# Performance work log

Hardware: AMD Instinct MI355X
Metric: run time of the kernel (lower is better)

The kernel has to match this reference:

```python
import jax, jax.numpy as jnp
import numpy as np

EMBED_DIM = 1280
NUM_HEADS = 20
HEAD_DIM = EMBED_DIM // NUM_HEADS
BSZ, SEQ = 4, 1500


def setup_inputs() -> dict:
    key = jax.random.key(0)
    ks = jax.random.split(key, 8)
    s = 1.0 / np.sqrt(EMBED_DIM)
    return {
        "hidden_states": jax.random.normal(ks[0], (BSZ, SEQ, EMBED_DIM), jnp.float32),
        "attention_mask": jnp.zeros((BSZ, 1, SEQ, SEQ), jnp.float32),
        "Wq": jax.random.normal(ks[1], (EMBED_DIM, EMBED_DIM), jnp.float32) * s,
        "bq": jax.random.normal(ks[2], (EMBED_DIM,), jnp.float32) * 0.01,
        "Wk": jax.random.normal(ks[3], (EMBED_DIM, EMBED_DIM), jnp.float32) * s,
        "Wv": jax.random.normal(ks[4], (EMBED_DIM, EMBED_DIM), jnp.float32) * s,
        "bv": jax.random.normal(ks[5], (EMBED_DIM,), jnp.float32) * 0.01,
        "Wo": jax.random.normal(ks[6], (EMBED_DIM, EMBED_DIM), jnp.float32) * s,
        "bo": jax.random.normal(ks[7], (EMBED_DIM,), jnp.float32) * 0.01,
    }


def _split_heads(x):
    b, s, _ = x.shape
    return x.reshape(b, s, NUM_HEADS, HEAD_DIM).transpose(0, 2, 1, 3)  # [b,h,s,d]


def reference(hidden_states, attention_mask, Wq, bq, Wk, Wv, bv, Wo, bo):
    scale = jnp.float32(HEAD_DIM) ** -0.5
    q = (hidden_states @ Wq.T + bq) * scale          # [b,s,e]
    k = hidden_states @ Wk.T                          # k_proj has no bias
    v = hidden_states @ Wv.T + bv
    q, k, v = _split_heads(q), _split_heads(k), _split_heads(v)
    attn = jnp.einsum("bhqd,bhkd->bhqk", q, k)       # [b,h,s,s]
    attn = attn + attention_mask
    attn = jax.nn.softmax(attn, axis=-1)
    out = jnp.einsum("bhqk,bhkd->bhqd", attn, v)     # [b,h,s,d]
    out = out.transpose(0, 2, 1, 3).reshape(hidden_states.shape)
    return out @ Wo.T + bo
```

## Files before the change

### kernel.cpp

```cpp
#include <hip/hip_runtime.h>

typedef unsigned short u16;
typedef unsigned long long u64;
using bf16x8 = __attribute__((ext_vector_type(8))) __bf16;
using f32x4  = __attribute__((ext_vector_type(4))) float;
using u32x2  = __attribute__((ext_vector_type(2))) unsigned;
using u32x4  = __attribute__((ext_vector_type(4))) unsigned;

#define AS1 __attribute__((address_space(1)))
#define AS3 __attribute__((address_space(3)))

__device__ __forceinline__ void glds16(const u16* g, u16* l) {
  __builtin_amdgcn_global_load_lds((AS1 void*)const_cast<u16*>(g), (AS3 void*)l, 16, 0, 0);
}

__device__ __forceinline__ u16 f2bf(float f) {
  unsigned u = __float_as_uint(f);
  u += 0x7FFFu + ((u >> 16) & 1u);
  return (u16)(u >> 16);
}
__device__ __forceinline__ ushort4 cvt4(float4 v) {
  return make_ushort4(f2bf(v.x), f2bf(v.y), f2bf(v.z), f2bf(v.w));
}

__device__ __forceinline__ unsigned cvt_pk_bf16(float lo, float hi) {
  unsigned r;
  asm("v_cvt_pk_bf16_f32 %0, %1, %2" : "=v"(r) : "v"(lo), "v"(hi));
  return r;
}

#if __has_builtin(__builtin_amdgcn_exp2f)
__device__ __forceinline__ float fexp2(float x) { return __builtin_amdgcn_exp2f(x); }
#else
__device__ __forceinline__ float fexp2(float x) { return exp2f(x); }
#endif

__device__ __forceinline__ void quad_swap(unsigned& x, unsigned& y) {
  u32x2 a = __builtin_amdgcn_permlane32_swap(x, y, false, false);
  u32x2 b = __builtin_amdgcn_permlane16_swap(a[0], a[1], false, false);
  x = b[0];
  y = b[1];
}

__device__ __forceinline__ float xquad_max(float x) {
  u32x2 a = __builtin_amdgcn_permlane16_swap(__float_as_uint(x), __float_as_uint(x), false, false);
  float y = fmaxf(__uint_as_float(a[0]), __uint_as_float(a[1]));
  u32x2 b = __builtin_amdgcn_permlane32_swap(__float_as_uint(y), __float_as_uint(y), false, false);
  return fmaxf(__uint_as_float(b[0]), __uint_as_float(b[1]));
}
__device__ __forceinline__ float xquad_sum(float x) {
  u32x2 a = __builtin_amdgcn_permlane16_swap(__float_as_uint(x), __float_as_uint(x), false, false);
  float y = __uint_as_float(a[0]) + __uint_as_float(a[1]);
  u32x2 b = __builtin_amdgcn_permlane32_swap(__float_as_uint(y), __float_as_uint(y), false, false);
  return __uint_as_float(b[0]) + __uint_as_float(b[1]);
}

__global__ __launch_bounds__(256) void cvt_kernel(const float4* __restrict__ hs,
    const float4* __restrict__ wq, const float4* __restrict__ wk,
    const float4* __restrict__ wv, const float4* __restrict__ wo, u16* __restrict__ dst) {
  const long stride = (long)gridDim.x * blockDim.x;
  for (long i = (long)blockIdx.x * blockDim.x + threadIdx.x; i < 3558400; i += stride) {
    const float4* src; long rel; u16* d;
    if (i < 1920000)      { src = hs; rel = i;           d = dst; }
    else if (i < 2329600) { src = wq; rel = i - 1920000; d = dst + 7680000; }
    else if (i < 2739200) { src = wk; rel = i - 2329600; d = dst + 9318400; }
    else if (i < 3148800) { src = wv; rel = i - 2739200; d = dst + 10956800; }
    else                  { src = wo; rel = i - 3148800; d = dst + 12595200; }
    *(ushort4*)(d + rel * 4) = cvt4(src[rel]);
  }
}

template <int MODE, typename OT>
__device__ __forceinline__ void gemm256(const u16* __restrict__ A, const u16* __restrict__ W,
                                        const float* __restrict__ bias, OT* __restrict__ out,
                                        float scale, int M, u16* lds, int m0, int n0) {
  constexpr int K = 1280;
  constexpr int NT = 20;
  const int tid = threadIdx.x, wid = tid >> 6, lane = tid & 63;
  const int lm = lane & 15, quad = lane >> 4;
  const int wr = wid >> 1, wc = wid & 1;

  f32x4 acc[4][4] = {};

  const int srow = tid >> 3, sslot = tid & 7;
  const int scol = (sslot ^ (srow & 7)) * 8;
  int r0 = m0 + srow;       r0 = r0 < M ? r0 : M - 1;
  int r1 = m0 + 64 + srow;  r1 = r1 < M ? r1 : M - 1;
  int r2 = m0 + 128 + srow; r2 = r2 < M ? r2 : M - 1;
  int r3 = m0 + 192 + srow; r3 = r3 < M ? r3 : M - 1;
  const u16* a0 = A + (size_t)r0 * K + scol;
  const u16* a1 = A + (size_t)r1 * K + scol;
  const u16* a2 = A + (size_t)r2 * K + scol;
  const u16* a3 = A + (size_t)r3 * K + scol;
  const u16* w0 = W + (size_t)(n0 + srow) * K + scol;
  const u16* w1 = W + (size_t)(n0 + 64 + srow) * K + scol;
  const int wdst = wid * 512;

  auto stage_p = [&](int t, int bsel2, int p) {
    u16* bb = lds + bsel2 * 24576;
    const int kt = t * 64;
    if (p == 0) {
      glds16(a0 + kt, bb + wdst);
      glds16(a1 + kt, bb + 4096 + wdst);
      glds16(a2 + kt, bb + 8192 + wdst);
    } else {
      glds16(a3 + kt, bb + 12288 + wdst);
      glds16(w0 + kt, bb + 16384 + wdst);
      glds16(w1 + kt, bb + 20480 + wdst);
    }
  };

  stage_p(0, 0, 0); stage_p(0, 0, 1);
  stage_p(1, 1, 0); stage_p(1, 1, 1);
  asm volatile("s_waitcnt vmcnt(6)" ::: "memory");
  __builtin_amdgcn_s_barrier();

  int bsel = 0;
  for (int t = 0; t < NT; ++t) {
    const u16* Ab = lds + bsel * 24576;
    const u16* Bb = Ab + 16384;
    const int b2 = bsel >= 1 ? bsel - 1 : 2;
    const bool pf = (t + 2) < NT;
#pragma unroll
    for (int kk = 0; kk < 2; ++kk) {
      const int co = ((kk * 4 + quad) ^ (lm & 7)) * 8;
      bf16x8 af[4], bfr[4];
#pragma unroll
      for (int i = 0; i < 4; ++i)
        af[i] = *(const bf16x8*)(Ab + (wr * 64 + i * 16 + lm) * 64 + co);
#pragma unroll
      for (int j = 0; j < 4; ++j)
        bfr[j] = *(const bf16x8*)(Bb + (wc * 64 + j * 16 + lm) * 64 + co);
      if (pf) stage_p(t + 2, b2, kk);
      __builtin_amdgcn_sched_barrier(0);
      __builtin_amdgcn_s_barrier();
      __builtin_amdgcn_s_setprio(1);
#pragma unroll
      for (int i = 0; i < 4; ++i)
#pragma unroll
        for (int j = 0; j < 4; ++j)
          acc[i][j] = __builtin_amdgcn_mfma_f32_16x16x32_bf16(af[i], bfr[j], acc[i][j], 0, 0, 0);
      __builtin_amdgcn_s_setprio(0);
      __builtin_amdgcn_s_barrier();
    }
    if (t + 1 < NT) {
      if (pf) asm volatile("s_waitcnt vmcnt(6)" ::: "memory");
      else    asm volatile("s_waitcnt vmcnt(0)" ::: "memory");
      __builtin_amdgcn_s_barrier();
    }
    bsel = bsel == 2 ? 0 : bsel + 1;
  }

  if constexpr (MODE == 2) {
    __syncthreads();
    u16* Ct = lds;
#pragma unroll
    for (int j = 0; j < 4; ++j) {
      const int col = wc * 64 + j * 16 + lm;
      const float bb = bias ? bias[n0 + col] : 0.0f;
#pragma unroll
      for (int i = 0; i < 4; ++i) {
        const int row = wr * 64 + i * 16 + quad * 4;
        ushort4 pk;
        pk.x = f2bf((acc[i][j][0] + bb) * scale);
        pk.y = f2bf((acc[i][j][1] + bb) * scale);
        pk.z = f2bf((acc[i][j][2] + bb) * scale);
        pk.w = f2bf((acc[i][j][3] + bb) * scale);
        *(ushort4*)(Ct + col * 264 + row) = pk;
      }
    }
    __syncthreads();
#pragma unroll
    for (int k = 0; k < 8; ++k) {
      const int c8 = tid + k * 512;
      const int col = c8 >> 5, rc = c8 & 31;
      const int grow0 = m0 + rc * 8;
      if (grow0 >= M) continue;
      const int gcol = n0 + col, hh = gcol >> 6, dd = gcol & 63;
      const u16* src = Ct + col * 264 + rc * 8;
      const int b0 = grow0 / 1500, b1 = (grow0 + 7) / 1500;
      if (b0 == b1) {
        const int s = grow0 - b0 * 1500;
        u16* dst = (u16*)out + ((size_t)((b0 * 20 + hh) * 64 + dd)) * 1504 + s;
        *(u64*)dst = *(const u64*)src;
        *(u64*)(dst + 4) = *(const u64*)(src + 4);
      } else {
#pragma unroll
        for (int r = 0; r < 8; ++r) {
          const int g = grow0 + r;
          const int bi2 = g / 1500, s2 = g - bi2 * 1500;
          ((u16*)out)[((size_t)((bi2 * 20 + hh) * 64 + dd)) * 1504 + s2] = src[r];
        }
      }
    }
  } else {
#pragma unroll
    for (int j = 0; j < 4; ++j) {
      const int col = n0 + wc * 64 + j * 16 + lm;
      const float bb = bias ? bias[col] : 0.0f;
      const int hh = col >> 6, dd = col & 63;
#pragma unroll
      for (int i = 0; i < 4; ++i) {
        const int row0 = m0 + wr * 64 + i * 16 + quad * 4;
#pragma unroll
        for (int r = 0; r < 4; ++r) {
          const int row = row0 + r;
          if (row < M) {
            const float v = (acc[i][j][r] + bb) * scale;
            if (MODE == 0) {
              out[(size_t)row * 1280 + col] = (OT)v;
            } else {
              const int bidx = row / 1500, s = row - bidx * 1500;
              out[((size_t)(bidx * 20 + hh) * 1500 + s) * 64 + dd] = (OT)f2bf(v);
            }
          }
        }
      }
    }
  }
}

__global__ __launch_bounds__(512, 2) void qkv_kernel(const u16* __restrict__ hs,
    const u16* __restrict__ Wq, const float* __restrict__ bq, const u16* __restrict__ Wk,
    const u16* __restrict__ Wv, const float* __restrict__ bv,
    u16* __restrict__ q_ws, u16* __restrict__ k_ws, u16* __restrict__ vt_ws, int M) {
  __shared__ __align__(16) u16 lds[3 * 24576];
  const int n = blockIdx.x;
  const int xcd = n & 7, j = n >> 3;
  const int x = xcd * 3 + (j % 3);
  const int yz = j / 3;
  const int y = yz % 10, z = yz / 10;
  const int m0 = x * 256, n0 = y * 128;
  if (z == 0)
    gemm256<1, u16>(hs, Wq, bq, q_ws, 0.18033688f, M, lds, m0, n0);
  else if (z == 1)
    gemm256<1, u16>(hs, Wk, nullptr, k_ws, 1.0f, M, lds, m0, n0);
  else
    gemm256<2, u16>(hs, Wv, bv, vt_ws, 1.0f, M, lds, m0, n0);
}

__global__ __launch_bounds__(512, 2) void out_kernel(const u16* __restrict__ attn,
    const u16* __restrict__ Wo, const float* __restrict__ bo, float* __restrict__ out, int M) {
  __shared__ __align__(16) u16 lds[3 * 24576];
  const int n = blockIdx.x;
  const int xcd = n & 7, j = n >> 3;
  const int x = xcd * 3 + (j % 3);
  const int y = j / 3;
  gemm256<0, float>(attn, Wo, bo, out, 1.0f, M, lds, x * 256, y * 128);
}

__global__ __launch_bounds__(256, 3) void attn_kernel(const u16* __restrict__ Qm,
    const u16* __restrict__ Km, const u16* __restrict__ Vtm, u16* __restrict__ Out) {
  const int n = blockIdx.x;
  const int xcd = n & 7, j = n >> 3;
  const int bh = xcd * 10 + (j % 10);
  const int qt = j / 10;
  const int b = bh / 20, h = bh % 20;
  const int tid = threadIdx.x, wid = tid >> 6, lane = tid & 63;
  const int lm = lane & 15, quad = lane >> 4;

  __shared__ __align__(16) u16 lds[3 * 8192];

  const u16* Qb = Qm + (size_t)bh * (1500 * 64);
  const u16* Kb = Km + (size_t)bh * (1500 * 64);
  const u16* Vb = Vtm + (size_t)bh * (64 * 1504);

  bf16x8 qf[2][2];
#pragma unroll
  for (int g = 0; g < 2; ++g) {
    int qrow = qt * 128 + wid * 32 + g * 16 + lm;
    if (qrow > 1499) qrow = 1499;
    qf[g][0] = *(const bf16x8*)(Qb + (size_t)qrow * 64 + quad * 8);
    qf[g][1] = *(const bf16x8*)(Qb + (size_t)qrow * 64 + 32 + quad * 8);
  }

  const int rr = tid >> 3, cc = tid & 7;
  const int s0 = (cc ^ (rr & 7)) * 8;

  auto stage = [&](int kt, int bi) {
    int kr0 = kt + rr;      if (kr0 > 1499) kr0 = 1499;
    int kr1 = kt + rr + 32; if (kr1 > 1499) kr1 = 1499;
    int vcol = kt + s0;     if (vcol > 1496) vcol = 1496;
    u16* lk = lds + bi * 8192 + wid * 512;
    u16* lv = lk + 4096;
    glds16(Kb + (size_t)kr0 * 64 + s0, lk);
    glds16(Kb + (size_t)kr1 * 64 + s0, lk + 2048);
    glds16(Vb + (size_t)rr * 1504 + vcol, lv);
    glds16(Vb + (size_t)(rr + 32) * 1504 + vcol, lv + 2048);
  };

  stage(0, 0);
  stage(64, 1);
  asm volatile("s_waitcnt vmcnt(4)" ::: "memory");
  __builtin_amdgcn_s_barrier();

  float m_s[2] = {-1e30f, -1e30f};
  float l_s[2] = {0.f, 0.f};
  f32x4 o_acc[2][4] = {};

  int bsel = 0;
  for (int it = 0; it < 24; ++it) {
    const u16* Kc = lds + bsel * 8192;
    const u16* Vc = Kc + 4096;
    if (it + 2 < 24) stage((it + 2) * 64, bsel >= 1 ? bsel - 1 : 2);

    f32x4 st[2][4] = {};
    __builtin_amdgcn_s_setprio(1);
#pragma unroll
    for (int kk = 0; kk < 2; ++kk) {
#pragma unroll
      for (int t = 0; t < 4; ++t) {
        const bf16x8 kf = *(const bf16x8*)(Kc + (t * 16 + lm) * 64 + (((kk * 4 + quad) ^ (lm & 7)) * 8));
        st[0][t] = __builtin_amdgcn_mfma_f32_16x16x32_bf16(kf, qf[0][kk], st[0][t], 0, 0, 0);
        st[1][t] = __builtin_amdgcn_mfma_f32_16x16x32_bf16(kf, qf[1][kk], st[1][t], 0, 0, 0);
      }
    }
    __builtin_amdgcn_s_setprio(0);
    if (it == 23) {
#pragma unroll
      for (int t = 0; t < 4; ++t)
#pragma unroll
        for (int r = 0; r < 4; ++r)
          if (t * 16 + quad * 4 + r >= 28) { st[0][t][r] = -1e30f; st[1][t][r] = -1e30f; }
    }

    bf16x8 pf[2][2];
#pragma unroll
    for (int g = 0; g < 2; ++g) {
      float a0 = fmaxf(fmaxf(st[g][0][0], st[g][0][1]), fmaxf(st[g][0][2], st[g][0][3]));
      float a1 = fmaxf(fmaxf(st[g][1][0], st[g][1][1]), fmaxf(st[g][1][2], st[g][1][3]));
      float a2 = fmaxf(fmaxf(st[g][2][0], st[g][2][1]), fmaxf(st[g][2][2], st[g][2][3]));
      float a3 = fmaxf(fmaxf(st[g][3][0], st[g][3][1]), fmaxf(st[g][3][2], st[g][3][3]));
      float rm = xquad_max(fmaxf(fmaxf(a0, a1), fmaxf(a2, a3)));

      if (!__all(rm - m_s[g] <= 8.0f)) {
        const float mn = fmaxf(m_s[g], rm);
        const float al = fexp2(m_s[g] - mn);
        m_s[g] = mn;
        l_s[g] *= al;
#pragma unroll
        for (int r = 0; r < 4; ++r) {
          const float ao = __shfl(al, quad * 4 + r);
#pragma unroll
          for (int t = 0; t < 4; ++t) o_acc[g][t][r] *= ao;
        }
      }
      const float mn = m_s[g];

      float rs = 0.f;
      unsigned A[4], B[4];
#pragma unroll
      for (int t = 0; t < 4; ++t) {
        const float p0 = fexp2(st[g][t][0] - mn);
        const float p1 = fexp2(st[g][t][1] - mn);
        const float p2 = fexp2(st[g][t][2] - mn);
        const float p3 = fexp2(st[g][t][3] - mn);
        rs += (p0 + p1) + (p2 + p3);
        A[t] = cvt_pk_bf16(p0, p1);
        B[t] = cvt_pk_bf16(p2, p3);
      }
      l_s[g] += xquad_sum(rs);

#pragma unroll
      for (int kk = 0; kk < 2; ++kk) {
        unsigned x0 = A[2 * kk], x1 = A[2 * kk + 1];
        quad_swap(x0, x1);
        unsigned y0 = B[2 * kk], y1 = B[2 * kk + 1];
        quad_swap(y0, y1);
        u32x4 w; w[0] = x0; w[1] = y0; w[2] = x1; w[3] = y1;
        pf[g][kk] = __builtin_bit_cast(bf16x8, w);
      }
    }

    __builtin_amdgcn_s_setprio(1);
#pragma unroll
    for (int kk = 0; kk < 2; ++kk) {
#pragma unroll
      for (int t = 0; t < 4; ++t) {
        const bf16x8 vf = *(const bf16x8*)(Vc + (t * 16 + lm) * 64 + (((kk * 4 + quad) ^ (lm & 7)) * 8));
        o_acc[0][t] = __builtin_amdgcn_mfma_f32_16x16x32_bf16(pf[0][kk], vf, o_acc[0][t], 0, 0, 0);
        o_acc[1][t] = __builtin_amdgcn_mfma_f32_16x16x32_bf16(pf[1][kk], vf, o_acc[1][t], 0, 0, 0);
      }
    }
    __builtin_amdgcn_s_setprio(0);

    if (it + 1 < 24) {
      if (it + 2 < 24) asm volatile("s_waitcnt vmcnt(4)" ::: "memory");
      else             asm volatile("s_waitcnt vmcnt(0)" ::: "memory");
      __builtin_amdgcn_s_barrier();
    }
    bsel = bsel == 2 ? 0 : bsel + 1;
  }

#pragma unroll
  for (int g = 0; g < 2; ++g)
#pragma unroll
    for (int r = 0; r < 4; ++r) {
      const float lr = __shfl(l_s[g], quad * 4 + r);
      const float inv = 1.0f / lr;
      const int qg = qt * 128 + wid * 32 + g * 16 + quad * 4 + r;
      if (qg < 1500) {
#pragma unroll
        for (int t = 0; t < 4; ++t)
          Out[((size_t)(b * 1500 + qg)) * 1280 + h * 64 + t * 16 + lm] =
              f2bf(o_acc[g][t][r] * inv);
      }
    }
}

extern "C" void kernel_launch(void* const* d_in, const int* in_sizes, int n_in,
                              void* d_out, int out_size, void* d_ws, size_t ws_size,
                              hipStream_t stream) {
  const float* hs = (const float*)d_in[0];
  const float* Wq = (const float*)d_in[2];
  const float* bq = (const float*)d_in[3];
  const float* Wk = (const float*)d_in[4];
  const float* Wv = (const float*)d_in[5];
  const float* bv = (const float*)d_in[6];
  const float* Wo = (const float*)d_in[7];
  const float* bo = (const float*)d_in[8];

  u16* cvt     = (u16*)d_ws;
  u16* hs_bf   = cvt;
  u16* Wq_bf   = cvt + 7680000;
  u16* Wk_bf   = cvt + 9318400;
  u16* Wv_bf   = cvt + 10956800;
  u16* Wo_bf   = cvt + 12595200;
  u16* q_ws    = cvt + 14233600;
  u16* k_ws    = q_ws + 7680000;
  u16* vt_ws   = k_ws + 7680000;
  u16* attn_ws = vt_ws + 7700480 + 64;
  const int M = 6000;

  hipLaunchKernelGGL(cvt_kernel, dim3(2048), dim3(256), 0, stream,
                     (const float4*)hs, (const float4*)Wq, (const float4*)Wk,
                     (const float4*)Wv, (const float4*)Wo, cvt);
  hipLaunchKernelGGL(qkv_kernel, dim3(720), dim3(512), 0, stream,
                     hs_bf, Wq_bf, bq, Wk_bf, Wv_bf, bv, q_ws, k_ws, vt_ws, M);
  hipLaunchKernelGGL(attn_kernel, dim3(960), dim3(256), 0, stream,
                     q_ws, k_ws, vt_ws, attn_ws);
  hipLaunchKernelGGL(out_kernel, dim3(240), dim3(512), 0, stream,
                     attn_ws, Wo_bf, bo, (float*)d_out, M);
}
```

Baseline: 312.5 us.

## Enlarge GEMM tiles to 256x256 with an 8-phase double-buffered pipeline

Replaces the 256x128 triple-buffered GEMM with a 256x256 tile. Each of 8 waves now computes 128x64 (8x4 MFMA accumulators), and loads are interleaved over four compute phases using two LDS buffers. This halves the grid sizes for the QKV and output projections, aiming to raise arithmetic intensity and reduce LDS/global traffic per FLOP. The cost is more accumulator registers, fewer blocks for the 256 CUs (360 and 120), and a V-transpose epilogue split into two column chunks.

Result: slower. 341.7 us (+9.3%).

```diff
diff --git a/kernel.cpp b/kernel.cpp
--- a/kernel.cpp
+++ b/kernel.cpp
@@ -71,125 +71,178 @@
 }
 
 template <int MODE, typename OT>
-__device__ __forceinline__ void gemm256(const u16* __restrict__ A, const u16* __restrict__ W,
-                                        const float* __restrict__ bias, OT* __restrict__ out,
-                                        float scale, int M, u16* lds, int m0, int n0) {
+__device__ __forceinline__ void gemm8p(const u16* __restrict__ A, const u16* __restrict__ W,
+                                       const float* __restrict__ bias, OT* __restrict__ out,
+                                       float scale, int M, u16* lds, int m0, int n0) {
   constexpr int K = 1280;
   constexpr int NT = 20;
   const int tid = threadIdx.x, wid = tid >> 6, lane = tid & 63;
   const int lm = lane & 15, quad = lane >> 4;
-  const int wr = wid >> 1, wc = wid & 1;
-
-  f32x4 acc[4][4] = {};
+  const int wr = wid >> 2, wc = wid & 3;
+
+  f32x4 acc[8][4] = {};
 
   const int srow = tid >> 3, sslot = tid & 7;
   const int scol = (sslot ^ (srow & 7)) * 8;
-  int r0 = m0 + srow;       r0 = r0 < M ? r0 : M - 1;
-  int r1 = m0 + 64 + srow;  r1 = r1 < M ? r1 : M - 1;
-  int r2 = m0 + 128 + srow; r2 = r2 < M ? r2 : M - 1;
-  int r3 = m0 + 192 + srow; r3 = r3 < M ? r3 : M - 1;
-  const u16* a0 = A + (size_t)r0 * K + scol;
-  const u16* a1 = A + (size_t)r1 * K + scol;
-  const u16* a2 = A + (size_t)r2 * K + scol;
-  const u16* a3 = A + (size_t)r3 * K + scol;
-  const u16* w0 = W + (size_t)(n0 + srow) * K + scol;
-  const u16* w1 = W + (size_t)(n0 + 64 + srow) * K + scol;
+  const u16* ap[4]; const u16* wp[4];
+#pragma unroll
+  for (int i = 0; i < 4; ++i) {
+    int ra = m0 + i * 64 + srow; ra = ra < M ? ra : M - 1;
+    ap[i] = A + (size_t)ra * K + scol;
+    wp[i] = W + (size_t)(n0 + i * 64 + srow) * K + scol;
+  }
   const int wdst = wid * 512;
 
-  auto stage_p = [&](int t, int bsel2, int p) {
-    u16* bb = lds + bsel2 * 24576;
+  auto stA = [&](int t, int b, int half) {
     const int kt = t * 64;
-    if (p == 0) {
-      glds16(a0 + kt, bb + wdst);
-      glds16(a1 + kt, bb + 4096 + wdst);
-      glds16(a2 + kt, bb + 8192 + wdst);
-    } else {
-      glds16(a3 + kt, bb + 12288 + wdst);
-      glds16(w0 + kt, bb + 16384 + wdst);
-      glds16(w1 + kt, bb + 20480 + wdst);
-    }
+    glds16(ap[2 * half] + kt,     lds + b * 32768 + (2 * half) * 4096 + wdst);
+    glds16(ap[2 * half + 1] + kt, lds + b * 32768 + (2 * half + 1) * 4096 + wdst);
   };
-
-  stage_p(0, 0, 0); stage_p(0, 0, 1);
-  stage_p(1, 1, 0); stage_p(1, 1, 1);
-  asm volatile("s_waitcnt vmcnt(6)" ::: "memory");
+  auto stB = [&](int t, int b, int half) {
+    const int kt = t * 64;
+    glds16(wp[2 * half] + kt,     lds + b * 32768 + 16384 + (2 * half) * 4096 + wdst);
+    glds16(wp[2 * half + 1] + kt, lds + b * 32768 + 16384 + (2 * half + 1) * 4096 + wdst);
+  };
+
+  stA(0, 0, 0); stA(0, 0, 1); stB(0, 0, 0); stB(0, 0, 1);
+  stA(1, 1, 0); stB(1, 1, 0);
+  asm volatile("s_waitcnt vmcnt(4)" ::: "memory");
   __builtin_amdgcn_s_barrier();
 
-  int bsel = 0;
   for (int t = 0; t < NT; ++t) {
-    const u16* Ab = lds + bsel * 24576;
+    const int b = t & 1;
+    const u16* Ab = lds + b * 32768;
     const u16* Bb = Ab + 16384;
-    const int b2 = bsel >= 1 ? bsel - 1 : 2;
-    const bool pf = (t + 2) < NT;
-#pragma unroll
-    for (int kk = 0; kk < 2; ++kk) {
-      const int co = ((kk * 4 + quad) ^ (lm & 7)) * 8;
-      bf16x8 af[4], bfr[4];
+    const int co0 = ((0 + quad) ^ (lm & 7)) * 8;
+    const int co1 = ((4 + quad) ^ (lm & 7)) * 8;
+    bf16x8 afh[2][4], bf[2][4];
+
+#pragma unroll
+    for (int i = 0; i < 4; ++i) {
+      afh[0][i] = *(const bf16x8*)(Ab + (wr * 128 + i * 16 + lm) * 64 + co0);
+      afh[1][i] = *(const bf16x8*)(Ab + (wr * 128 + i * 16 + lm) * 64 + co1);
+    }
+#pragma unroll
+    for (int j = 0; j < 2; ++j) {
+      bf[0][j] = *(const bf16x8*)(Bb + (wc * 64 + j * 16 + lm) * 64 + co0);
+      bf[1][j] = *(const bf16x8*)(Bb + (wc * 64 + j * 16 + lm) * 64 + co1);
+    }
+    if (t + 1 < NT) stA(t + 1, b ^ 1, 1);
+    __builtin_amdgcn_sched_barrier(0);
+    __builtin_amdgcn_s_barrier();
+    __builtin_amdgcn_s_setprio(1);
+#pragma unroll
+    for (int kk = 0; kk < 2; ++kk)
 #pragma unroll
       for (int i = 0; i < 4; ++i)
-        af[i] = *(const bf16x8*)(Ab + (wr * 64 + i * 16 + lm) * 64 + co);
-#pragma unroll
-      for (int j = 0; j < 4; ++j)
-        bfr[j] = *(const bf16x8*)(Bb + (wc * 64 + j * 16 + lm) * 64 + co);
-      if (pf) stage_p(t + 2, b2, kk);
-      __builtin_amdgcn_sched_barrier(0);
-      __builtin_amdgcn_s_barrier();
-      __builtin_amdgcn_s_setprio(1);
+#pragma unroll
+        for (int j = 0; j < 2; ++j)
+          acc[i][j] = __builtin_amdgcn_mfma_f32_16x16x32_bf16(afh[kk][i], bf[kk][j], acc[i][j], 0, 0, 0);
+    __builtin_amdgcn_s_setprio(0);
+    __builtin_amdgcn_s_barrier();
+
+#pragma unroll
+    for (int j = 2; j < 4; ++j) {
+      bf[0][j] = *(const bf16x8*)(Bb + (wc * 64 + j * 16 + lm) * 64 + co0);
+      bf[1][j] = *(const bf16x8*)(Bb + (wc * 64 + j * 16 + lm) * 64 + co1);
+    }
+    if (t + 1 < NT) stB(t + 1, b ^ 1, 1);
+    __builtin_amdgcn_sched_barrier(0);
+    __builtin_amdgcn_s_barrier();
+    __builtin_amdgcn_s_setprio(1);
+#pragma unroll
+    for (int kk = 0; kk < 2; ++kk)
 #pragma unroll
       for (int i = 0; i < 4; ++i)
 #pragma unroll
-        for (int j = 0; j < 4; ++j)
-          acc[i][j] = __builtin_amdgcn_mfma_f32_16x16x32_bf16(af[i], bfr[j], acc[i][j], 0, 0, 0);
-      __builtin_amdgcn_s_setprio(0);
-      __builtin_amdgcn_s_barrier();
-    }
+        for (int j = 2; j < 4; ++j)
+          acc[i][j] = __builtin_amdgcn_mfma_f32_16x16x32_bf16(afh[kk][i], bf[kk][j], acc[i][j], 0, 0, 0);
+    __builtin_amdgcn_s_setprio(0);
+    __builtin_amdgcn_s_barrier();
+
+#pragma unroll
+    for (int i = 0; i < 4; ++i) {
+      afh[0][i] = *(const bf16x8*)(Ab + (wr * 128 + (i + 4) * 16 + lm) * 64 + co0);
+      afh[1][i] = *(const bf16x8*)(Ab + (wr * 128 + (i + 4) * 16 + lm) * 64 + co1);
+    }
+    if (t + 2 < NT) stA(t + 2, b, 0);
+    __builtin_amdgcn_sched_barrier(0);
+    __builtin_amdgcn_s_barrier();
+    __builtin_amdgcn_s_setprio(1);
+#pragma unroll
+    for (int kk = 0; kk < 2; ++kk)
+#pragma unroll
+      for (int i = 0; i < 4; ++i)
+#pragma unroll
+        for (int j = 0; j < 2; ++j)
+          acc[i + 4][j] = __builtin_amdgcn_mfma_f32_16x16x32_bf16(afh[kk][i], bf[kk][j], acc[i + 4][j], 0, 0, 0);
+    __builtin_amdgcn_s_setprio(0);
+    __builtin_amdgcn_s_barrier();
+
+    if (t + 2 < NT) stB(t + 2, b, 0);
+    __builtin_amdgcn_sched_barrier(0);
+    __builtin_amdgcn_s_barrier();
+    __builtin_amdgcn_s_setprio(1);
+#pragma unroll
+    for (int kk = 0; kk < 2; ++kk)
+#pragma unroll
+      for (int i = 0; i < 4; ++i)
+#pragma unroll
+        for (int j = 2; j < 4; ++j)
+          acc[i + 4][j] = __builtin_amdgcn_mfma_f32_16x16x32_bf16(afh[kk][i], bf[kk][j], acc[i + 4][j], 0, 0, 0);
+    __builtin_amdgcn_s_setprio(0);
     if (t + 1 < NT) {
-      if (pf) asm volatile("s_waitcnt vmcnt(6)" ::: "memory");
-      else    asm volatile("s_waitcnt vmcnt(0)" ::: "memory");
-      __builtin_amdgcn_s_barrier();
-    }
-    bsel = bsel == 2 ? 0 : bsel + 1;
+      if (t + 2 < NT) asm volatile("s_waitcnt vmcnt(4)" ::: "memory");
+      else            asm volatile("s_waitcnt vmcnt(0)" ::: "memory");
+    }
+    __builtin_amdgcn_s_barrier();
   }
 
   if constexpr (MODE == 2) {
-    __syncthreads();
     u16* Ct = lds;
 #pragma unroll
-    for (int j = 0; j < 4; ++j) {
-      const int col = wc * 64 + j * 16 + lm;
-      const float bb = bias ? bias[n0 + col] : 0.0f;
-#pragma unroll
-      for (int i = 0; i < 4; ++i) {
-        const int row = wr * 64 + i * 16 + quad * 4;
-        ushort4 pk;
-        pk.x = f2bf((acc[i][j][0] + bb) * scale);
-        pk.y = f2bf((acc[i][j][1] + bb) * scale);
-        pk.z = f2bf((acc[i][j][2] + bb) * scale);
-        pk.w = f2bf((acc[i][j][3] + bb) * scale);
-        *(ushort4*)(Ct + col * 264 + row) = pk;
-      }
-    }
-    __syncthreads();
-#pragma unroll
-    for (int k = 0; k < 8; ++k) {
-      const int c8 = tid + k * 512;
-      const int col = c8 >> 5, rc = c8 & 31;
-      const int grow0 = m0 + rc * 8;
-      if (grow0 >= M) continue;
-      const int gcol = n0 + col, hh = gcol >> 6, dd = gcol & 63;
-      const u16* src = Ct + col * 264 + rc * 8;
-      const int b0 = grow0 / 1500, b1 = (grow0 + 7) / 1500;
-      if (b0 == b1) {
-        const int s = grow0 - b0 * 1500;
-        u16* dst = (u16*)out + ((size_t)((b0 * 20 + hh) * 64 + dd)) * 1504 + s;
-        *(u64*)dst = *(const u64*)src;
-        *(u64*)(dst + 4) = *(const u64*)(src + 4);
-      } else {
-#pragma unroll
-        for (int r = 0; r < 8; ++r) {
-          const int g = grow0 + r;
-          const int bi2 = g / 1500, s2 = g - bi2 * 1500;
-          ((u16*)out)[((size_t)((bi2 * 20 + hh) * 64 + dd)) * 1504 + s2] = src[r];
+    for (int ch = 0; ch < 2; ++ch) {
+      __syncthreads();
+      if ((wc >> 1) == ch) {
+        const int colbase = (wc & 1) * 64;
+#pragma unroll
+        for (int j = 0; j < 4; ++j) {
+          const int col = colbase + j * 16 + lm;
+          const float bb = bias ? bias[n0 + ch * 128 + col] : 0.0f;
+#pragma unroll
+          for (int i = 0; i < 8; ++i) {
+            const int row = wr * 128 + i * 16 + quad * 4;
+            ushort4 pk;
+            pk.x = f2bf((acc[i][j][0] + bb) * scale);
+            pk.y = f2bf((acc[i][j][1] + bb) * scale);
+            pk.z = f2bf((acc[i][j][2] + bb) * scale);
+            pk.w = f2bf((acc[i][j][3] + bb) * scale);
+            *(ushort4*)(Ct + col * 264 + row) = pk;
+          }
+        }
+      }
+      __syncthreads();
+#pragma unroll
+      for (int k = 0; k < 8; ++k) {
+        const int c8 = tid + k * 512;
+        const int col = c8 >> 5, rc = c8 & 31;
+        const int grow0 = m0 + rc * 8;
+        if (grow0 >= M) continue;
+        const int gcol = n0 + ch * 128 + col, hh = gcol >> 6, dd = gcol & 63;
+        const u16* src = Ct + col * 264 + rc * 8;
+        const int b0 = grow0 / 1500, b1 = (grow0 + 7) / 1500;
+        if (b0 == b1) {
+          const int s = grow0 - b0 * 1500;
+          u16* dst = (u16*)out + ((size_t)((b0 * 20 + hh) * 64 + dd)) * 1504 + s;
+          *(u64*)dst = *(const u64*)src;
+          *(u64*)(dst + 4) = *(const u64*)(src + 4);
+        } else {
+#pragma unroll
+          for (int r = 0; r < 8; ++r) {
+            const int g = grow0 + r;
+            const int bi2 = g / 1500, s2 = g - bi2 * 1500;
+            ((u16*)out)[((size_t)((bi2 * 20 + hh) * 64 + dd)) * 1504 + s2] = src[r];
+          }
         }
       }
     }
@@ -200,8 +253,8 @@
       const float bb = bias ? bias[col] : 0.0f;
       const int hh = col >> 6, dd = col & 63;
 #pragma unroll
-      for (int i = 0; i < 4; ++i) {
-        const int row0 = m0 + wr * 64 + i * 16 + quad * 4;
+      for (int i = 0; i < 8; ++i) {
+        const int row0 = m0 + wr * 128 + i * 16 + quad * 4;
 #pragma unroll
         for (int r = 0; r < 4; ++r) {
           const int row = row0 + r;
@@ -224,29 +277,29 @@
     const u16* __restrict__ Wq, const float* __restrict__ bq, const u16* __restrict__ Wk,
     const u16* __restrict__ Wv, const float* __restrict__ bv,
     u16* __restrict__ q_ws, u16* __restrict__ k_ws, u16* __restrict__ vt_ws, int M) {
-  __shared__ __align__(16) u16 lds[3 * 24576];
+  __shared__ __align__(16) u16 lds[2 * 32768];
   const int n = blockIdx.x;
   const int xcd = n & 7, j = n >> 3;
   const int x = xcd * 3 + (j % 3);
   const int yz = j / 3;
-  const int y = yz % 10, z = yz / 10;
-  const int m0 = x * 256, n0 = y * 128;
+  const int y = yz % 5, z = yz / 5;
+  const int m0 = x * 256, n0 = y * 256;
   if (z == 0)
-    gemm256<1, u16>(hs, Wq, bq, q_ws, 0.18033688f, M, lds, m0, n0);
+    gemm8p<1, u16>(hs, Wq, bq, q_ws, 0.18033688f, M, lds, m0, n0);
   else if (z == 1)
-    gemm256<1, u16>(hs, Wk, nullptr, k_ws, 1.0f, M, lds, m0, n0);
+    gemm8p<1, u16>(hs, Wk, nullptr, k_ws, 1.0f, M, lds, m0, n0);
   else
-    gemm256<2, u16>(hs, Wv, bv, vt_ws, 1.0f, M, lds, m0, n0);
+    gemm8p<2, u16>(hs, Wv, bv, vt_ws, 1.0f, M, lds, m0, n0);
 }
 
 __global__ __launch_bounds__(512, 2) void out_kernel(const u16* __restrict__ attn,
     const u16* __restrict__ Wo, const float* __restrict__ bo, float* __restrict__ out, int M) {
-  __shared__ __align__(16) u16 lds[3 * 24576];
+  __shared__ __align__(16) u16 lds[2 * 32768];
   const int n = blockIdx.x;
   const int xcd = n & 7, j = n >> 3;
   const int x = xcd * 3 + (j % 3);
   const int y = j / 3;
-  gemm256<0, float>(attn, Wo, bo, out, 1.0f, M, lds, x * 256, y * 128);
+  gemm8p<0, float>(attn, Wo, bo, out, 1.0f, M, lds, x * 256, y * 256);
 }
 
 __global__ __launch_bounds__(256, 3) void attn_kernel(const u16* __restrict__ Qm,
@@ -435,10 +488,10 @@
   hipLaunchKernelGGL(cvt_kernel, dim3(2048), dim3(256), 0, stream,
                      (const float4*)hs, (const float4*)Wq, (const float4*)Wk,
                      (const float4*)Wv, (const float4*)Wo, cvt);
-  hipLaunchKernelGGL(qkv_kernel, dim3(720), dim3(512), 0, stream,
+  hipLaunchKernelGGL(qkv_kernel, dim3(360), dim3(512), 0, stream,
                      hs_bf, Wq_bf, bq, Wk_bf, Wv_bf, bv, q_ws, k_ws, vt_ws, M);
   hipLaunchKernelGGL(attn_kernel, dim3(960), dim3(256), 0, stream,
                      q_ws, k_ws, vt_ws, attn_ws);
-  hipLaunchKernelGGL(out_kernel, dim3(240), dim3(512), 0, stream,
+  hipLaunchKernelGGL(out_kernel, dim3(120), dim3(512), 0, stream,
                      attn_ws, Wo_bf, bo, (float*)d_out, M);
 }
```
